# Performance work log

Hardware: AMD Instinct MI355X
Metric: run time of the kernel (lower is better)

## Reference

```python
import jax, jax.numpy as jnp
import numpy as np
from jax import lax

N, C, A, K, D = 2, 256, 3, 20, 256  # batch, channels, anchors, topk person cells, rn_fc_dim
BOX = 4
SIZES = [(80, 128), (40, 64), (20, 32), (10, 16)]
DN = ('NCHW', 'OIHW', 'NCHW')


def _conv(x, w, b):
    return lax.conv_general_dilated(x, w, (1, 1), 'SAME', dimension_numbers=DN) + b[None, :, None, None]


def setup_inputs() -> dict:
    key = jax.random.key(0)
    ks = iter(jax.random.split(key, 40))
    d = {}
    for i, (h, w) in enumerate(SIZES):
        d['feat%d' % i] = jax.random.normal(next(ks), (N, C, h, w), jnp.float32)
    def wfn(shape, s=0.05):
        return jax.random.normal(next(ks), shape, jnp.float32) * s
    d['pc1_w'] = wfn((C, C, 3, 3)); d['pc1_b'] = jnp.zeros((C,), jnp.float32)
    d['pc2_w'] = wfn((C, C, 3, 3)); d['pc2_b'] = jnp.zeros((C,), jnp.float32)
    d['oc1_w'] = wfn((C, C, 3, 3)); d['oc1_b'] = jnp.zeros((C,), jnp.float32)
    d['oc2_w'] = wfn((C, C, 3, 3)); d['oc2_b'] = jnp.zeros((C,), jnp.float32)
    # relation-net FCs: first takes concat(object, person) -> 2C in
    d['rn1_w'] = wfn((D, 2 * C)); d['rn1_b'] = jnp.zeros((D,), jnp.float32)
    d['rn2_w'] = wfn((D, D)); d['rn2_b'] = jnp.zeros((D,), jnp.float32)
    # heads
    d['pl_w'] = wfn((A, C, 1, 1), 0.01); d['pl_b'] = jnp.zeros((A,), jnp.float32)
    d['pd_w'] = wfn((A * BOX, C, 1, 1), 0.01); d['pd_b'] = jnp.zeros((A * BOX,), jnp.float32)
    d['ol_w'] = wfn((A, D), 0.01); d['ol_b'] = jnp.zeros((A,), jnp.float32)
    d['od_w'] = wfn((A * BOX, C, 1, 1), 0.01); d['od_b'] = jnp.zeros((A * BOX,), jnp.float32)
    return d


def _find_top_cells(hidden, logits, topk):
    hid_l, sc_l = [], []
    for h_map, lg in zip(hidden, logits):
        n, c, H, W = h_map.shape
        cell_scores = jnp.max(lg, axis=1).reshape(n, -1)          # (N, HW)
        ts, tc = lax.top_k(cell_scores, topk)                      # (N, K)
        hv = h_map.reshape(n, c, -1)                               # (N, C, HW)
        hid_l.append(jnp.take_along_axis(hv, tc[:, None, :], axis=2))  # (N, C, K)
        sc_l.append(ts)
    scores = jnp.concatenate(sc_l, axis=1)                         # (N, L*K)
    hid = jnp.concatenate(hid_l, axis=2)                           # (N, C, L*K)
    _, keep = lax.top_k(scores, topk)
    return jnp.take_along_axis(hid, keep[:, None, :], axis=2)      # (N, C, K)


def _forward(feats, pc1_w, pc1_b, pc2_w, pc2_b, oc1_w, oc1_b, oc2_w, oc2_b,
             rn1_w, rn1_b, rn2_w, rn2_b, pl_w, pl_b, pd_w, pd_b, ol_w, ol_b, od_w, od_b):
    # person branch
    p_hid, p_log, p_del = [], [], []
    for x in feats:
        x = jax.nn.relu(_conv(x, pc1_w, pc1_b))
        x = jax.nn.relu(_conv(x, pc2_w, pc2_b))
        p_hid.append(x)
        p_log.append(_conv(x, pl_w, pl_b))
        p_del.append(_conv(x, pd_w, pd_b))
    topk_person = _find_top_cells(p_hid, p_log, K)                 # (N, C, K)
    pf = topk_person.transpose(0, 2, 1)                            # (N, K, C)
    # object branch: fc1(concat(o, p)) == o @ Wo.T + p @ Wp.T + b (concat order: object first)
    Wo, Wp = rn1_w[:, :C], rn1_w[:, C:]
    p_proj = jnp.einsum('nkc,dc->nkd', pf, Wp) + rn1_b             # (N, K, D)
    o_log, o_del = [], []
    for x in feats:
        n, _, H, W = x.shape
        y = jax.nn.relu(_conv(x, oc1_w, oc1_b))
        y = jax.nn.relu(_conv(y, oc2_w, oc2_b))
        o_del.append(_conv(y, od_w, od_b))
        yf = y.reshape(n, C, H * W).transpose(0, 2, 1)             # (N, HW, C)
        o_proj = jnp.einsum('nsc,dc->nsd', yf, Wo)                 # (N, HW, D)
        h = jax.nn.relu(o_proj[:, :, None, :] + p_proj[:, None, :, :])  # (N, HW, K, D)
        h = h.sum(axis=2)                                          # (N, HW, D)
        h = jax.nn.relu(jnp.einsum('nsd,ed->nse', h, rn2_w) + rn2_b)
        ol = jnp.einsum('nsd,ad->nsa', h, ol_w) + ol_b             # (N, HW, A)
        o_log.append(ol.transpose(0, 2, 1).reshape(n, A, H, W))
    return tuple(p_log) + tuple(p_del) + tuple(o_log) + tuple(o_del)


def reference(feat0, feat1, feat2, feat3, pc1_w, pc1_b, pc2_w, pc2_b, oc1_w, oc1_b, oc2_w, oc2_b,
              rn1_w, rn1_b, rn2_w, rn2_b, pl_w, pl_b, pd_w, pd_b, ol_w, ol_b, od_w, od_b):
    return _forward([feat0, feat1, feat2, feat3], pc1_w, pc1_b, pc2_w, pc2_b, oc1_w, oc1_b,
                    oc2_w, oc2_b, rn1_w, rn1_b, rn2_w, rn2_b, pl_w, pl_b, pd_w, pd_b,
                    ol_w, ol_b, od_w, od_b)
```

## Files before the change

kernel.cpp:

```cpp
#include <hip/hip_runtime.h>
#include <cstdint>
#include <cstddef>

typedef __bf16 bf16x8 __attribute__((ext_vector_type(8)));
typedef float  f32x16 __attribute__((ext_vector_type(16)));

union U16 { bf16x8 v; uint4 q; };
union U8  { __bf16 h[4]; unsigned long long u; };

typedef __attribute__((address_space(1))) const unsigned char gas_t;
typedef __attribute__((address_space(3))) unsigned char las_t;
__device__ __forceinline__ void async16(const void* g, void* l) {
    __builtin_amdgcn_global_load_lds((gas_t*)g, (las_t*)l, 16, 0, 0);
}

__device__ __forceinline__ int lvl256(int bx) {
    return (bx < 40) ? 0 : (bx < 50) ? 1 : (bx < 53) ? 2 : 3;
}
__device__ __forceinline__ int tbase256(int lv) {
    return (lv == 0) ? 0 : (lv == 1) ? 40 : (lv == 2) ? 50 : 53;
}
__device__ __forceinline__ size_t loffE(int lv) {
    return (lv == 0) ? 0 : (lv == 1) ? 5242880 : (lv == 2) ? 6553600 : 6881280;
}
__device__ __forceinline__ size_t plog_off(int lv) {
    return (lv == 0) ? 0 : (lv == 1) ? 61440 : (lv == 2) ? 76800 : 80640;
}
__device__ __forceinline__ size_t pdel_off(int lv) {
    return (lv == 0) ? 81600 : (lv == 1) ? 327360 : (lv == 2) ? 388800 : 404160;
}
__device__ __forceinline__ size_t olog_off(int lv) {
    return (lv == 0) ? 408000 : (lv == 1) ? 469440 : (lv == 2) ? 484800 : 488640;
}
__device__ __forceinline__ size_t odel_off(int lv) {
    return (lv == 0) ? 489600 : (lv == 1) ? 735360 : (lv == 2) ? 796800 : 812160;
}
__device__ __forceinline__ int soff_l(int lv) {
    return (lv == 0) ? 0 : (lv == 1) ? 20480 : (lv == 2) ? 25600 : 26880;
}

__global__ __launch_bounds__(256) void prep_all_k(
    const float* f0, const float* f1, const float* f2, const float* f3,
    const float* pc1w, const float* pc2w, const float* oc1w, const float* oc2w,
    const float* __restrict__ rn1w, const float* __restrict__ rn2w,
    const float* __restrict__ olw,
    __bf16* __restrict__ wtap, float* __restrict__ WpT,
    __bf16* __restrict__ Wo16, __bf16* __restrict__ rn216,
    __bf16* __restrict__ olw32,
    unsigned* __restrict__ zrow32, __bf16* __restrict__ x16)
{
    __shared__ float f[2304];
    int bid = blockIdx.x, tid = threadIdx.x;
    if (bid < 1024) {
        int which = bid >> 8, co = bid & 255;
        const float* srcw = (which == 0) ? pc1w : (which == 1) ? pc2w
                          : (which == 2) ? oc1w : oc2w;
        const float* src = srcw + (size_t)co * 2304;
        for (int i = tid; i < 2304; i += 256) f[i] = src[i];
        __syncthreads();
        __bf16* dst = wtap + (size_t)which * 589824;
        int cg = co >> 6, co64 = co & 63;
        for (int u = tid; u < 288; u += 256) {
            int t = u >> 5, rest = u & 31, c16 = rest >> 1, hf = rest & 1;
            int ci0 = c16 * 16 + hf * 8;
            U16 v;
#pragma unroll
            for (int j = 0; j < 8; ++j) v.v[j] = (__bf16)f[(ci0 + j) * 9 + t];
            *(uint4*)&dst[(size_t)t * 65536 + c16 * 4096 + cg * 1024 + hf * 512 + co64 * 8] = v.q;
        }
    } else if (bid < 1280) {
        int d = bid - 1024, c = tid;
        WpT[c * 256 + d] = rn1w[(size_t)d * 512 + 256 + c];
        Wo16[((c >> 4) * 256 + d) * 16 + (c & 15)] = (__bf16)rn1w[(size_t)d * 512 + c];
        rn216[((c >> 4) * 256 + d) * 16 + (c & 15)] = (__bf16)rn2w[(size_t)d * 256 + c];
        if (d == 0) zrow32[c] = 0u;
    } else if (bid < 3008) {
        int u = bid - 1280;
        int bx = u >> 5, rr = u & 31, n = rr >> 4, ch = rr & 15;
        int lv = lvl256(bx);
        int HW = 10240 >> (2 * lv);
        int p = (bx - tbase256(lv)) * 256 + tid;
        if (p >= HW) return;
        const float* fp = (lv == 0) ? f0 : (lv == 1) ? f1 : (lv == 2) ? f2 : f3;
        const float* src = fp + (size_t)n * 256 * HW + (size_t)ch * 16 * HW + p;
        U16 a, b;
#pragma unroll
        for (int j = 0; j < 8; ++j) a.v[j] = (__bf16)src[(size_t)j * HW];
#pragma unroll
        for (int j = 0; j < 8; ++j) b.v[j] = (__bf16)src[(size_t)(8 + j) * HW];
        size_t o = loffE(lv) + (size_t)n * HW * 256 + (((size_t)ch * HW + p) << 4);
        *(uint4*)&x16[o] = a.q;
        *(uint4*)&x16[o + 8] = b.q;
    } else {
        int e16 = bid - 3008;
        for (int idx = tid; idx < 512; idx += 256) {
            int co = idx >> 4, j = idx & 15;
            float v = (co < 3) ? olw[co * 256 + e16 * 16 + j] : 0.f;
            olw32[e16 * 512 + co * 16 + j] = (__bf16)v;
        }
    }
}

__global__ __launch_bounds__(256, 3) void conv3x3_v6(
    const __bf16* __restrict__ inA, const __bf16* __restrict__ inB,
    const __bf16* __restrict__ wtA, const __bf16* __restrict__ wtB,
    const float* __restrict__ bA, const float* __restrict__ bB,
    const __bf16* __restrict__ zrow,
    __bf16* __restrict__ outA, __bf16* __restrict__ outB, int mode)
{
    __shared__ __bf16 Asm[2][9216];

    const int id = blockIdx.x;
    const int r8 = id & 7, q = id >> 3;
    int by, br, n, tile;
    if (mode == 0) {
        by = q & 3; br = (q >> 2) & 1;
        int T = ((q >> 3) << 3) + r8; if (T >= 108) return;
        n = T & 1; tile = T >> 1;
    } else if (mode == 1) {
        by = q & 3;
        int T2 = ((q >> 2) << 3) + r8; if (T2 >= 216) return;
        br = T2 & 1; n = (T2 >> 1) & 1; tile = T2 >> 2;
    } else {
        by = q & 3; br = 0;
        int T = ((q >> 2) << 3) + r8; if (T >= 108) return;
        n = T & 1; tile = T >> 1;
    }

    const int tid = threadIdx.x;
    const __bf16* in16 = br ? inB : inA;
    const __bf16* wt = br ? wtB : wtA;
    const float* bias = br ? bB : bA;
    __bf16* outp = br ? outB : outA;

    const int lv = lvl256(tile);
    const int lg2W = 7 - lv;
    const int W = 1 << lg2W, H = 80 >> lv;
    const int HW = 10240 >> (2 * lv);
    const size_t ioff = loffE(lv) + (size_t)n * HW * 256;
    const __bf16* inb = in16 + ioff;

    const int sp0 = (tile - tbase256(lv)) << 8;
    const int npix = min(256, HW - sp0);

    const int w = tid >> 6, l64 = tid & 63;
    const int lane = l64 & 31, half = l64 >> 5;
    const int pix0 = (w << 6) + lane, pix1 = pix0 + 32;
    const int cobase = by << 6;

    int boff0[9], boff1[9];
    {
        const int y0 = sp0 >> lg2W;
        const int py0 = pix0 >> lg2W, px0 = pix0 & (W - 1);
        const int py1 = pix1 >> lg2W, px1 = pix1 & (W - 1);
#pragma unroll
        for (int dy = 0; dy < 3; ++dy)
#pragma unroll
            for (int dx = 0; dx < 3; ++dx) {
                int t = dy * 3 + dx;
                int gy0 = y0 + py0 + dy - 1, gx0 = px0 + dx - 1;
                boff0[t] = ((unsigned)gy0 < (unsigned)H && (unsigned)gx0 < (unsigned)W)
                           ? (((gy0 << lg2W) + gx0) * 32 + half * 16) : -1;
                int gy1 = y0 + py1 + dy - 1, gx1 = px1 + dx - 1;
                boff1[t] = ((unsigned)gy1 < (unsigned)H && (unsigned)gx1 < (unsigned)W)
                           ? (((gy1 << lg2W) + gx1) * 32 + half * 16) : -1;
            }
    }
    const __bf16* zp = zrow + (half << 3);

    const char* wtb = (const char*)wt + (by * 2048);
    auto stage = [&](int c16, int buf) {
        const char* base = wtb + (size_t)c16 * 8192;
        for (int u = w; u < 18; u += 4) {
            int t = u >> 1, hf = u & 1;
            async16(base + (size_t)t * 131072 + hf * 1024 + l64 * 16,
                    &Asm[buf][u * 512]);
        }
    };

    f32x16 acc00 = {}, acc01 = {}, acc10 = {}, acc11 = {};

    stage(0, 0);
    int buf = 0;
    for (int c16 = 0; c16 < 16; ++c16) {
        __syncthreads();
        if (c16 < 15) stage(c16 + 1, buf ^ 1);
        const char* curB = (const char*)inb + (size_t)c16 * HW * 32;
        const __bf16* Ab = &Asm[buf][0];
#pragma unroll
        for (int t = 0; t < 9; ++t) {
            bf16x8 a0 = *(const bf16x8*)&Ab[t * 1024 + half * 512 + lane * 8];
            bf16x8 a1 = *(const bf16x8*)&Ab[t * 1024 + half * 512 + 256 + lane * 8];
            const __bf16* q0 = (boff0[t] >= 0) ? (const __bf16*)(curB + boff0[t]) : zp;
            const __bf16* q1 = (boff1[t] >= 0) ? (const __bf16*)(curB + boff1[t]) : zp;
            bf16x8 b0 = *(const bf16x8*)q0;
            bf16x8 b1 = *(const bf16x8*)q1;
            acc00 = __builtin_amdgcn_mfma_f32_32x32x16_bf16(a0, b0, acc00, 0, 0, 0);
            acc01 = __builtin_amdgcn_mfma_f32_32x32x16_bf16(a0, b1, acc01, 0, 0, 0);
            acc10 = __builtin_amdgcn_mfma_f32_32x32x16_bf16(a1, b0, acc10, 0, 0, 0);
            acc11 = __builtin_amdgcn_mfma_f32_32x32x16_bf16(a1, b1, acc11, 0, 0, 0);
        }
        buf ^= 1;
    }
    const int pixg0 = sp0 + pix0, pixg1 = sp0 + pix1;
    const bool ok0 = (pix0 < npix), ok1 = (pix1 < npix);
#pragma unroll
    for (int b = 0; b < 2; ++b) {
        const f32x16& A0 = b ? acc10 : acc00;
        const f32x16& A1 = b ? acc11 : acc01;
#pragma unroll
        for (int qq = 0; qq < 4; ++qq) {
            int co0 = cobase + b * 32 + qq * 8 + half * 4;
            float4 bq = *(const float4*)&bias[co0];
            U8 v0, v1;
            v0.h[0] = (__bf16)fmaxf(A0[qq * 4 + 0] + bq.x, 0.f);
            v0.h[1] = (__bf16)fmaxf(A0[qq * 4 + 1] + bq.y, 0.f);
            v0.h[2] = (__bf16)fmaxf(A0[qq * 4 + 2] + bq.z, 0.f);
            v0.h[3] = (__bf16)fmaxf(A0[qq * 4 + 3] + bq.w, 0.f);
            v1.h[0] = (__bf16)fmaxf(A1[qq * 4 + 0] + bq.x, 0.f);
            v1.h[1] = (__bf16)fmaxf(A1[qq * 4 + 1] + bq.y, 0.f);
            v1.h[2] = (__bf16)fmaxf(A1[qq * 4 + 2] + bq.z, 0.f);
            v1.h[3] = (__bf16)fmaxf(A1[qq * 4 + 3] + bq.w, 0.f);
            size_t base = ioff + (((size_t)(co0 >> 4) * HW) << 4) + (co0 & 15);
            if (ok0) *(unsigned long long*)&outp[base + ((size_t)pixg0 << 4)] = v0.u;
            if (ok1) *(unsigned long long*)&outp[base + ((size_t)pixg1 << 4)] = v1.u;
        }
    }
}

__global__ __launch_bounds__(256) void heads_k(
    const __bf16* __restrict__ h16p, const __bf16* __restrict__ h16o,
    const float* __restrict__ plw, const float* __restrict__ plb,
    const float* __restrict__ pdw, const float* __restrict__ pdb,
    const float* __restrict__ odw, const float* __restrict__ odb,
    float* __restrict__ out, float* __restrict__ scores)
{
    int bx = blockIdx.x, n = blockIdx.y, br = blockIdx.z;
    int lv = lvl256(bx);
    int HW = 10240 >> (2 * lv);
    int p = (bx - tbase256(lv)) * 256 + threadIdx.x;
    if (p >= HW) return;
    size_t ioff = loffE(lv) + (size_t)n * HW * 256;
    if (br == 0) {
        float acc[15];
#pragma unroll
        for (int a = 0; a < 15; ++a) acc[a] = 0.f;
        for (int ch = 0; ch < 16; ++ch) {
            size_t base = ioff + (((size_t)ch * HW + p) << 4);
            bf16x8 v0 = *(const bf16x8*)&h16p[base];
            bf16x8 v1 = *(const bf16x8*)&h16p[base + 8];
#pragma unroll
            for (int j = 0; j < 16; ++j) {
                float vv = (j < 8) ? (float)v0[j] : (float)v1[j - 8];
                int c = ch * 16 + j;
#pragma unroll
                for (int a = 0; a < 3; ++a)  acc[a]     = fmaf(plw[a * 256 + c], vv, acc[a]);
#pragma unroll
                for (int a = 0; a < 12; ++a) acc[3 + a] = fmaf(pdw[a * 256 + c], vv, acc[3 + a]);
            }
        }
        float sc = -INFINITY;
#pragma unroll
        for (int a = 0; a < 3; ++a) {
            float lg = acc[a] + plb[a];
            out[plog_off(lv) + ((size_t)n * 3 + a) * HW + p] = lg;
            sc = fmaxf(sc, lg);
        }
        scores[soff_l(lv) + (size_t)n * HW + p] = sc;
#pragma unroll
        for (int a = 0; a < 12; ++a)
            out[pdel_off(lv) + ((size_t)n * 12 + a) * HW + p] = acc[3 + a] + pdb[a];
    } else {
        float acc[12];
#pragma unroll
        for (int a = 0; a < 12; ++a) acc[a] = 0.f;
        for (int ch = 0; ch < 16; ++ch) {
            size_t base = ioff + (((size_t)ch * HW + p) << 4);
            bf16x8 v0 = *(const bf16x8*)&h16o[base];
            bf16x8 v1 = *(const bf16x8*)&h16o[base + 8];
#pragma unroll
            for (int j = 0; j < 16; ++j) {
                float vv = (j < 8) ? (float)v0[j] : (float)v1[j - 8];
                int c = ch * 16 + j;
#pragma unroll
                for (int a = 0; a < 12; ++a) acc[a] = fmaf(odw[a * 256 + c], vv, acc[a]);
            }
        }
#pragma unroll
        for (int a = 0; a < 12; ++a)
            out[odel_off(lv) + ((size_t)n * 12 + a) * HW + p] = acc[a] + odb[a];
    }
}

__global__ __launch_bounds__(256) void topk_lvl_k(
    const float* __restrict__ scores, float* __restrict__ lv_sc,
    int* __restrict__ lv_ix)
{
    int l = blockIdx.x, n = blockIdx.y;
    int HW = 10240 >> (2 * l);
    const float* sp = scores + soff_l(l) + (size_t)n * HW;
    int tid = threadIdx.x;
    __shared__ float sc[10240];
    __shared__ float wv4[4];
    __shared__ int wi4[4];
    __shared__ int bcast;
    for (int i = tid; i < HW; i += 256) sc[i] = sp[i];
    __syncthreads();
    float bv = -INFINITY; int bi = 0x7fffffff;
    for (int i = tid; i < HW; i += 256)
        if (sc[i] > bv) { bv = sc[i]; bi = i; }
    const int w = tid >> 6, lane = tid & 63;
    for (int r = 0; r < 20; ++r) {
        float cv = bv; int ci = bi;
#pragma unroll
        for (int off = 32; off > 0; off >>= 1) {
            float ov = __shfl_xor(cv, off);
            int oi = __shfl_xor(ci, off);
            if (ov > cv || (ov == cv && oi < ci)) { cv = ov; ci = oi; }
        }
        if (lane == 0) { wv4[w] = cv; wi4[w] = ci; }
        __syncthreads();
        if (tid == 0) {
            float mv = wv4[0]; int mi = wi4[0];
#pragma unroll
            for (int j = 1; j < 4; ++j)
                if (wv4[j] > mv || (wv4[j] == mv && wi4[j] < mi)) { mv = wv4[j]; mi = wi4[j]; }
            bcast = mi;
            int idx = (n * 4 + l) * 20 + r;
            lv_sc[idx] = mv;
            lv_ix[idx] = mi;
        }
        __syncthreads();
        int mi = bcast;
        if ((mi & 255) == tid) {
            sc[mi] = -INFINITY;
            bv = -INFINITY; bi = 0x7fffffff;
            for (int i = tid; i < HW; i += 256)
                if (sc[i] > bv) { bv = sc[i]; bi = i; }
        }
    }
}

__global__ __launch_bounds__(256) void sel_pproj_k(
    const float* __restrict__ lv_sc, const int* __restrict__ lv_ix,
    const __bf16* __restrict__ h16p, const float* __restrict__ WpT,
    const float* __restrict__ rn1b, float* __restrict__ pp)
{
    int n = blockIdx.x, tid = threadIdx.x;
    __shared__ int selL[20], selC[20];
    __shared__ float pfL[5120];
    __shared__ float wv2[2];
    __shared__ int wi2[2];
    __shared__ int bcast;
    float bv = -INFINITY; int bi = 0x7fffffff;
    if (tid < 80) { bv = lv_sc[n * 80 + tid]; bi = tid; }
    const int w = tid >> 6, lane = tid & 63;
    for (int r = 0; r < 20; ++r) {
        float cv = bv; int ci = bi;
#pragma unroll
        for (int off = 32; off > 0; off >>= 1) {
            float ov = __shfl_xor(cv, off);
            int oi = __shfl_xor(ci, off);
            if (ov > cv || (ov == cv && oi < ci)) { cv = ov; ci = oi; }
        }
        if (lane == 0 && w < 2) { wv2[w] = cv; wi2[w] = ci; }
        __syncthreads();
        if (tid == 0) {
            float mv = wv2[0]; int mi = wi2[0];
            if (wv2[1] > mv || (wv2[1] == mv && wi2[1] < mi)) { mv = wv2[1]; mi = wi2[1]; }
            bcast = mi;
            selL[r] = mi / 20;
            selC[r] = lv_ix[n * 80 + mi];
        }
        __syncthreads();
        if (bcast == bi) bv = -INFINITY;
    }
    for (int t = tid; t < 5120; t += 256) {
        int k = t >> 8, c = t & 255;
        int l = selL[k], cell = selC[k];
        int HW = 10240 >> (2 * l);
        pfL[k * 256 + c] =
            (float)h16p[loffE(l) + (size_t)n * HW * 256 +
                        (((size_t)(c >> 4) * HW + cell) << 4) + (c & 15)];
    }
    __syncthreads();
    float acc[20];
    float bb = rn1b[tid];
#pragma unroll
    for (int k = 0; k < 20; ++k) acc[k] = bb;
    for (int c = 0; c < 256; ++c) {
        float wv = WpT[c * 256 + tid];
#pragma unroll
        for (int k = 0; k < 20; ++k) acc[k] = fmaf(pfL[k * 256 + c], wv, acc[k]);
    }
#pragma unroll
    for (int k = 0; k < 20; ++k)
        pp[(size_t)n * 5120 + k * 256 + tid] = acc[k];
}

__global__ __launch_bounds__(256) void orel_k(
    const __bf16* __restrict__ H16o, const __bf16* __restrict__ Wo16,
    const __bf16* __restrict__ rn216, const __bf16* __restrict__ olw32,
    const float* __restrict__ pp, const float* __restrict__ rn2b,
    const float* __restrict__ olb, float* __restrict__ out)
{
    __shared__ __bf16 hb[16 * 64 * 24];
    __shared__ __bf16 pp16[5120];
    __shared__ float red[768];
    const int tid = threadIdx.x;
    const int n = blockIdx.y;
    int bx = blockIdx.x;
    int lv = (bx < 160) ? 0 : (bx < 200) ? 1 : (bx < 210) ? 2 : 3;
    int tb = (lv == 0) ? 0 : (lv == 1) ? 160 : (lv == 2) ? 200 : 210;
    int HW = 10240 >> (2 * lv);
    size_t yoff = loffE(lv) + (size_t)n * HW * 256;
    int p0 = (bx - tb) << 6;
    int npix = min(64, HW - p0);

    {
        const float* ps = pp + (size_t)n * 5120;
        for (int i = tid; i < 1280; i += 256) {
            float4 f = *(const float4*)&ps[i * 4];
            U8 v;
            v.h[0] = (__bf16)f.x; v.h[1] = (__bf16)f.y;
            v.h[2] = (__bf16)f.z; v.h[3] = (__bf16)f.w;
            *(unsigned long long*)&pp16[i * 4] = v.u;
        }
    }
    __syncthreads();

    const int w = tid >> 6, l64 = tid & 63;
    const int lane = l64 & 31, half = l64 >> 5;
    const int dbase = w << 6;

    f32x16 acc00 = {}, acc01 = {}, acc10 = {}, acc11 = {};
    for (int c16 = 0; c16 < 16; ++c16) {
        bf16x8 a0 = *(const bf16x8*)&Wo16[(((c16 << 8) + dbase + lane) << 4) + (half << 3)];
        bf16x8 a1 = *(const bf16x8*)&Wo16[(((c16 << 8) + dbase + 32 + lane) << 4) + (half << 3)];
        bf16x8 b0 = *(const bf16x8*)&H16o[yoff + (((size_t)c16 * HW + p0 + lane) << 4) + (half << 3)];
        bf16x8 b1 = *(const bf16x8*)&H16o[yoff + (((size_t)c16 * HW + p0 + 32 + lane) << 4) + (half << 3)];
        acc00 = __builtin_amdgcn_mfma_f32_32x32x16_bf16(a0, b0, acc00, 0, 0, 0);
        acc01 = __builtin_amdgcn_mfma_f32_32x32x16_bf16(a0, b1, acc01, 0, 0, 0);
        acc10 = __builtin_amdgcn_mfma_f32_32x32x16_bf16(a1, b0, acc10, 0, 0, 0);
        acc11 = __builtin_amdgcn_mfma_f32_32x32x16_bf16(a1, b1, acc11, 0, 0, 0);
    }
#pragma unroll
    for (int b = 0; b < 2; ++b) {
        const f32x16& A0 = b ? acc10 : acc00;
        const f32x16& A1 = b ? acc11 : acc01;
#pragma unroll
        for (int q = 0; q < 4; ++q) {
            int d0 = dbase + b * 32 + q * 8 + half * 4;
            float h0[4] = {0.f, 0.f, 0.f, 0.f}, h1[4] = {0.f, 0.f, 0.f, 0.f};
            for (int k = 0; k < 20; ++k) {
                U8 pk;
                pk.u = *(const unsigned long long*)&pp16[k * 256 + d0];
#pragma unroll
                for (int j = 0; j < 4; ++j) {
                    float pkv = (float)pk.h[j];
                    h0[j] += fmaxf(A0[q * 4 + j] + pkv, 0.f);
                    h1[j] += fmaxf(A1[q * 4 + j] + pkv, 0.f);
                }
            }
            U8 v0, v1;
#pragma unroll
            for (int j = 0; j < 4; ++j) { v0.h[j] = (__bf16)h0[j]; v1.h[j] = (__bf16)h1[j]; }
            *(unsigned long long*)&hb[((d0 >> 4) * 64 + lane) * 24 + (d0 & 15)] = v0.u;
            *(unsigned long long*)&hb[((d0 >> 4) * 64 + 32 + lane) * 24 + (d0 & 15)] = v1.u;
        }
    }
    __syncthreads();
    f32x16 e00 = {}, e01 = {}, e10 = {}, e11 = {};
    for (int d16 = 0; d16 < 16; ++d16) {
        bf16x8 a0 = *(const bf16x8*)&rn216[(((d16 << 8) + dbase + lane) << 4) + (half << 3)];
        bf16x8 a1 = *(const bf16x8*)&rn216[(((d16 << 8) + dbase + 32 + lane) << 4) + (half << 3)];
        bf16x8 b0 = *(const bf16x8*)&hb[(d16 * 64 + lane) * 24 + (half << 3)];
        bf16x8 b1 = *(const bf16x8*)&hb[(d16 * 64 + 32 + lane) * 24 + (half << 3)];
        e00 = __builtin_amdgcn_mfma_f32_32x32x16_bf16(a0, b0, e00, 0, 0, 0);
        e01 = __builtin_amdgcn_mfma_f32_32x32x16_bf16(a0, b1, e01, 0, 0, 0);
        e10 = __builtin_amdgcn_mfma_f32_32x32x16_bf16(a1, b0, e10, 0, 0, 0);
        e11 = __builtin_amdgcn_mfma_f32_32x32x16_bf16(a1, b1, e11, 0, 0, 0);
    }
    __syncthreads();
#pragma unroll
    for (int b = 0; b < 2; ++b) {
        const f32x16& A0 = b ? e10 : e00;
        const f32x16& A1 = b ? e11 : e01;
#pragma unroll
        for (int q = 0; q < 4; ++q) {
            int e0 = dbase + b * 32 + q * 8 + half * 4;
            float4 bb = *(const float4*)&rn2b[e0];
            U8 v0, v1;
            v0.h[0] = (__bf16)fmaxf(A0[q * 4 + 0] + bb.x, 0.f);
            v0.h[1] = (__bf16)fmaxf(A0[q * 4 + 1] + bb.y, 0.f);
            v0.h[2] = (__bf16)fmaxf(A0[q * 4 + 2] + bb.z, 0.f);
            v0.h[3] = (__bf16)fmaxf(A0[q * 4 + 3] + bb.w, 0.f);
            v1.h[0] = (__bf16)fmaxf(A1[q * 4 + 0] + bb.x, 0.f);
            v1.h[1] = (__bf16)fmaxf(A1[q * 4 + 1] + bb.y, 0.f);
            v1.h[2] = (__bf16)fmaxf(A1[q * 4 + 2] + bb.z, 0.f);
            v1.h[3] = (__bf16)fmaxf(A1[q * 4 + 3] + bb.w, 0.f);
            *(unsigned long long*)&hb[((e0 >> 4) * 64 + lane) * 24 + (e0 & 15)] = v0.u;
            *(unsigned long long*)&hb[((e0 >> 4) * 64 + 32 + lane) * 24 + (e0 & 15)] = v1.u;
        }
    }
    __syncthreads();
    f32x16 ol0 = {}, ol1 = {};
#pragma unroll
    for (int j = 0; j < 4; ++j) {
        int e16 = w * 4 + j;
        bf16x8 a = *(const bf16x8*)&olw32[e16 * 512 + lane * 16 + (half << 3)];
        bf16x8 b0 = *(const bf16x8*)&hb[(e16 * 64 + lane) * 24 + (half << 3)];
        bf16x8 b1 = *(const bf16x8*)&hb[(e16 * 64 + 32 + lane) * 24 + (half << 3)];
        ol0 = __builtin_amdgcn_mfma_f32_32x32x16_bf16(a, b0, ol0, 0, 0, 0);
        ol1 = __builtin_amdgcn_mfma_f32_32x32x16_bf16(a, b1, ol1, 0, 0, 0);
    }
    if (half == 0) {
#pragma unroll
        for (int r = 0; r < 3; ++r) {
            red[(r * 64 + lane) * 4 + w] = ol0[r];
            red[(r * 64 + lane + 32) * 4 + w] = ol1[r];
        }
    }
    __syncthreads();
    if (tid < 192) {
        int a = tid >> 6, px = tid & 63;
        if (px < npix) {
            float4 p4 = *(const float4*)&red[(a * 64 + px) * 4];
            out[olog_off(lv) + ((size_t)n * 3 + a) * HW + p0 + px] =
                olb[a] + p4.x + p4.y + p4.z + p4.w;
        }
    }
}

extern "C" void kernel_launch(void* const* d_in, const int* in_sizes, int n_in,
                              void* d_out, int out_size, void* d_ws, size_t ws_size,
                              hipStream_t stream)
{
    const float* feat[4] = {(const float*)d_in[0], (const float*)d_in[1],
                            (const float*)d_in[2], (const float*)d_in[3]};
    const float* pc1w = (const float*)d_in[4];  const float* pc1b = (const float*)d_in[5];
    const float* pc2w = (const float*)d_in[6];  const float* pc2b = (const float*)d_in[7];
    const float* oc1w = (const float*)d_in[8];  const float* oc1b = (const float*)d_in[9];
    const float* oc2w = (const float*)d_in[10]; const float* oc2b = (const float*)d_in[11];
    const float* rn1w = (const float*)d_in[12]; const float* rn1b = (const float*)d_in[13];
    const float* rn2w = (const float*)d_in[14]; const float* rn2b = (const float*)d_in[15];
    const float* plw  = (const float*)d_in[16]; const float* plb  = (const float*)d_in[17];
    const float* pdw  = (const float*)d_in[18]; const float* pdb  = (const float*)d_in[19];
    const float* olw  = (const float*)d_in[20]; const float* olb  = (const float*)d_in[21];
    const float* odw  = (const float*)d_in[22]; const float* odb  = (const float*)d_in[23];

    float* ws = (float*)d_ws;
    __bf16* bufA = (__bf16*)(ws);
    __bf16* bufB = (__bf16*)(ws + 3481600);
    __bf16* bufC = (__bf16*)(ws + 6963200);
    __bf16* wtap = (__bf16*)(ws + 10444800);
    __bf16* wt_pc1 = wtap;
    __bf16* wt_pc2 = wtap + 589824;
    __bf16* wt_oc1 = wtap + 2 * 589824;
    __bf16* wt_oc2 = wtap + 3 * 589824;
    __bf16* Wo16  = (__bf16*)(ws + 11624448);
    __bf16* rn216 = (__bf16*)(ws + 11657216);
    float* WpT    = ws + 11689984;
    float* scores = ws + 11755520;
    float* lv_sc  = ws + 11783040;
    int*   lv_ix  = (int*)(ws + 11783200);
    __bf16* olw32 = (__bf16*)(ws + 11783360);
    float* pp     = ws + 11793280;
    __bf16* zrow  = (__bf16*)(ws + 11803520);
    __bf16* bufD  = (__bf16*)(ws + 11803904);
    float* out    = (float*)d_out;

    const bool merged = ws_size >= (size_t)(11803904 + 3481600) * 4;

    hipLaunchKernelGGL(prep_all_k, dim3(3024), dim3(256), 0, stream,
                       feat[0], feat[1], feat[2], feat[3],
                       pc1w, pc2w, oc1w, oc2w, rn1w, rn2w, olw,
                       wtap, WpT, Wo16, rn216, olw32, (unsigned*)zrow, bufA);

    hipLaunchKernelGGL(conv3x3_v6, dim3(896), dim3(256), 0, stream,
                       bufA, bufA, wt_pc1, wt_oc1, pc1b, oc1b, zrow,
                       bufB, bufC, 0);

    __bf16* h16o;
    if (merged) {
        hipLaunchKernelGGL(conv3x3_v6, dim3(864), dim3(256), 0, stream,
                           bufB, bufC, wt_pc2, wt_oc2, pc2b, oc2b, zrow,
                           bufA, bufD, 1);
        h16o = bufD;
    } else {
        hipLaunchKernelGGL(conv3x3_v6, dim3(448), dim3(256), 0, stream,
                           bufB, bufB, wt_pc2, wt_pc2, pc2b, pc2b, zrow,
                           bufA, bufA, 2);
        hipLaunchKernelGGL(conv3x3_v6, dim3(448), dim3(256), 0, stream,
                           bufC, bufC, wt_oc2, wt_oc2, oc2b, oc2b, zrow,
                           bufB, bufB, 2);
        h16o = bufB;
    }

    hipLaunchKernelGGL(heads_k, dim3(54, 2, 2), dim3(256), 0, stream,
                       bufA, h16o, plw, plb, pdw, pdb, odw, odb, out, scores);

    hipLaunchKernelGGL(topk_lvl_k, dim3(4, 2), dim3(256), 0, stream,
                       scores, lv_sc, lv_ix);
    hipLaunchKernelGGL(sel_pproj_k, dim3(2), dim3(256), 0, stream,
                       lv_sc, lv_ix, bufA, WpT, rn1b, pp);

    hipLaunchKernelGGL(orel_k, dim3(213, 2), dim3(256), 0, stream,
                       h16o, Wo16, rn216, olw32, pp, rn2b, olb, out);
}
```

Before: 497.2 us.

## Fuse object delta head into orel kernel via MFMA and raise conv occupancy hint

The object-branch 1x1 delta head moves out of the scalar-FMA heads kernel and into orel_k. There it runs as extra MFMA ops on the same activation fragments already loaded for the Wo projection, using a new bf16 padded weight buffer built in prep. This removes a second full read of the object hidden map and halves the heads grid. Separately, the conv launch bound goes from 3 to 4 waves, which may force register spills. The delta head now runs in bf16 inside a single warp, so that warp does more work than the others.

```diff
diff --git a/kernel.cpp b/kernel.cpp
--- a/kernel.cpp
+++ b/kernel.cpp
@@ -43,10 +43,10 @@
     const float* f0, const float* f1, const float* f2, const float* f3,
     const float* pc1w, const float* pc2w, const float* oc1w, const float* oc2w,
     const float* __restrict__ rn1w, const float* __restrict__ rn2w,
-    const float* __restrict__ olw,
+    const float* __restrict__ olw, const float* __restrict__ odw,
     __bf16* __restrict__ wtap, float* __restrict__ WpT,
     __bf16* __restrict__ Wo16, __bf16* __restrict__ rn216,
-    __bf16* __restrict__ olw32,
+    __bf16* __restrict__ olw32, __bf16* __restrict__ odw32,
     unsigned* __restrict__ zrow32, __bf16* __restrict__ x16)
 {
     __shared__ float f[2304];
@@ -91,17 +91,24 @@
         size_t o = loffE(lv) + (size_t)n * HW * 256 + (((size_t)ch * HW + p) << 4);
         *(uint4*)&x16[o] = a.q;
         *(uint4*)&x16[o + 8] = b.q;
-    } else {
+    } else if (bid < 3024) {
         int e16 = bid - 3008;
         for (int idx = tid; idx < 512; idx += 256) {
             int co = idx >> 4, j = idx & 15;
             float v = (co < 3) ? olw[co * 256 + e16 * 16 + j] : 0.f;
             olw32[e16 * 512 + co * 16 + j] = (__bf16)v;
         }
-    }
-}
-
-__global__ __launch_bounds__(256, 3) void conv3x3_v6(
+    } else {
+        int c16 = bid - 3024;
+        for (int idx = tid; idx < 512; idx += 256) {
+            int co = idx >> 4, j = idx & 15;
+            float v = (co < 12) ? odw[co * 256 + c16 * 16 + j] : 0.f;
+            odw32[c16 * 512 + co * 16 + j] = (__bf16)v;
+        }
+    }
+}
+
+__global__ __launch_bounds__(256, 4) void conv3x3_v6(
     const __bf16* __restrict__ inA, const __bf16* __restrict__ inB,
     const __bf16* __restrict__ wtA, const __bf16* __restrict__ wtB,
     const float* __restrict__ bA, const float* __restrict__ bB,
@@ -229,67 +236,45 @@
 }
 
 __global__ __launch_bounds__(256) void heads_k(
-    const __bf16* __restrict__ h16p, const __bf16* __restrict__ h16o,
+    const __bf16* __restrict__ h16p,
     const float* __restrict__ plw, const float* __restrict__ plb,
     const float* __restrict__ pdw, const float* __restrict__ pdb,
-    const float* __restrict__ odw, const float* __restrict__ odb,
     float* __restrict__ out, float* __restrict__ scores)
 {
-    int bx = blockIdx.x, n = blockIdx.y, br = blockIdx.z;
+    int bx = blockIdx.x, n = blockIdx.y;
     int lv = lvl256(bx);
     int HW = 10240 >> (2 * lv);
     int p = (bx - tbase256(lv)) * 256 + threadIdx.x;
     if (p >= HW) return;
     size_t ioff = loffE(lv) + (size_t)n * HW * 256;
-    if (br == 0) {
-        float acc[15];
-#pragma unroll
-        for (int a = 0; a < 15; ++a) acc[a] = 0.f;
-        for (int ch = 0; ch < 16; ++ch) {
-            size_t base = ioff + (((size_t)ch * HW + p) << 4);
-            bf16x8 v0 = *(const bf16x8*)&h16p[base];
-            bf16x8 v1 = *(const bf16x8*)&h16p[base + 8];
-#pragma unroll
-            for (int j = 0; j < 16; ++j) {
-                float vv = (j < 8) ? (float)v0[j] : (float)v1[j - 8];
-                int c = ch * 16 + j;
-#pragma unroll
-                for (int a = 0; a < 3; ++a)  acc[a]     = fmaf(plw[a * 256 + c], vv, acc[a]);
-#pragma unroll
-                for (int a = 0; a < 12; ++a) acc[3 + a] = fmaf(pdw[a * 256 + c], vv, acc[3 + a]);
-            }
-        }
-        float sc = -INFINITY;
-#pragma unroll
-        for (int a = 0; a < 3; ++a) {
-            float lg = acc[a] + plb[a];
-            out[plog_off(lv) + ((size_t)n * 3 + a) * HW + p] = lg;
-            sc = fmaxf(sc, lg);
-        }
-        scores[soff_l(lv) + (size_t)n * HW + p] = sc;
-#pragma unroll
-        for (int a = 0; a < 12; ++a)
-            out[pdel_off(lv) + ((size_t)n * 12 + a) * HW + p] = acc[3 + a] + pdb[a];
-    } else {
-        float acc[12];
-#pragma unroll
-        for (int a = 0; a < 12; ++a) acc[a] = 0.f;
-        for (int ch = 0; ch < 16; ++ch) {
-            size_t base = ioff + (((size_t)ch * HW + p) << 4);
-            bf16x8 v0 = *(const bf16x8*)&h16o[base];
-            bf16x8 v1 = *(const bf16x8*)&h16o[base + 8];
-#pragma unroll
-            for (int j = 0; j < 16; ++j) {
-                float vv = (j < 8) ? (float)v0[j] : (float)v1[j - 8];
-                int c = ch * 16 + j;
-#pragma unroll
-                for (int a = 0; a < 12; ++a) acc[a] = fmaf(odw[a * 256 + c], vv, acc[a]);
-            }
-        }
-#pragma unroll
-        for (int a = 0; a < 12; ++a)
-            out[odel_off(lv) + ((size_t)n * 12 + a) * HW + p] = acc[a] + odb[a];
-    }
+    float acc[15];
+#pragma unroll
+    for (int a = 0; a < 15; ++a) acc[a] = 0.f;
+    for (int ch = 0; ch < 16; ++ch) {
+        size_t base = ioff + (((size_t)ch * HW + p) << 4);
+        bf16x8 v0 = *(const bf16x8*)&h16p[base];
+        bf16x8 v1 = *(const bf16x8*)&h16p[base + 8];
+#pragma unroll
+        for (int j = 0; j < 16; ++j) {
+            float vv = (j < 8) ? (float)v0[j] : (float)v1[j - 8];
+            int c = ch * 16 + j;
+#pragma unroll
+            for (int a = 0; a < 3; ++a)  acc[a]     = fmaf(plw[a * 256 + c], vv, acc[a]);
+#pragma unroll
+            for (int a = 0; a < 12; ++a) acc[3 + a] = fmaf(pdw[a * 256 + c], vv, acc[3 + a]);
+        }
+    }
+    float sc = -INFINITY;
+#pragma unroll
+    for (int a = 0; a < 3; ++a) {
+        float lg = acc[a] + plb[a];
+        out[plog_off(lv) + ((size_t)n * 3 + a) * HW + p] = lg;
+        sc = fmaxf(sc, lg);
+    }
+    scores[soff_l(lv) + (size_t)n * HW + p] = sc;
+#pragma unroll
+    for (int a = 0; a < 12; ++a)
+        out[pdel_off(lv) + ((size_t)n * 12 + a) * HW + p] = acc[3 + a] + pdb[a];
 }
 
 __global__ __launch_bounds__(256) void topk_lvl_k(
@@ -401,8 +386,9 @@
 __global__ __launch_bounds__(256) void orel_k(
     const __bf16* __restrict__ H16o, const __bf16* __restrict__ Wo16,
     const __bf16* __restrict__ rn216, const __bf16* __restrict__ olw32,
-    const float* __restrict__ pp, const float* __restrict__ rn2b,
-    const float* __restrict__ olb, float* __restrict__ out)
+    const __bf16* __restrict__ odw32, const float* __restrict__ pp,
+    const float* __restrict__ rn2b, const float* __restrict__ olb,
+    const float* __restrict__ odb, float* __restrict__ out)
 {
     __shared__ __bf16 hb[16 * 64 * 24];
     __shared__ __bf16 pp16[5120];
@@ -434,6 +420,7 @@
     const int dbase = w << 6;
 
     f32x16 acc00 = {}, acc01 = {}, acc10 = {}, acc11 = {};
+    f32x16 od0 = {}, od1 = {};
     for (int c16 = 0; c16 < 16; ++c16) {
         bf16x8 a0 = *(const bf16x8*)&Wo16[(((c16 << 8) + dbase + lane) << 4) + (half << 3)];
         bf16x8 a1 = *(const bf16x8*)&Wo16[(((c16 << 8) + dbase + 32 + lane) << 4) + (half << 3)];
@@ -443,6 +430,23 @@
         acc01 = __builtin_amdgcn_mfma_f32_32x32x16_bf16(a0, b1, acc01, 0, 0, 0);
         acc10 = __builtin_amdgcn_mfma_f32_32x32x16_bf16(a1, b0, acc10, 0, 0, 0);
         acc11 = __builtin_amdgcn_mfma_f32_32x32x16_bf16(a1, b1, acc11, 0, 0, 0);
+        if (w == 0) {
+            bf16x8 ao = *(const bf16x8*)&odw32[(c16 << 9) + lane * 16 + (half << 3)];
+            od0 = __builtin_amdgcn_mfma_f32_32x32x16_bf16(ao, b0, od0, 0, 0, 0);
+            od1 = __builtin_amdgcn_mfma_f32_32x32x16_bf16(ao, b1, od1, 0, 0, 0);
+        }
+    }
+    if (w == 0) {
+        size_t ob = odel_off(lv) + (size_t)n * 12 * HW + p0;
+#pragma unroll
+        for (int reg = 0; reg < 16; ++reg) {
+            int row = (reg & 3) + ((reg >> 2) << 3) + (half << 2);
+            if (row < 12) {
+                float bv = odb[row];
+                if (lane < npix)      out[ob + (size_t)row * HW + lane] = od0[reg] + bv;
+                if (32 + lane < npix) out[ob + (size_t)row * HW + 32 + lane] = od1[reg] + bv;
+            }
+        }
     }
 #pragma unroll
     for (int b = 0; b < 2; ++b) {
@@ -565,6 +569,7 @@
     float* lv_sc  = ws + 11783040;
     int*   lv_ix  = (int*)(ws + 11783200);
     __bf16* olw32 = (__bf16*)(ws + 11783360);
+    __bf16* odw32 = (__bf16*)(ws + 11787456);
     float* pp     = ws + 11793280;
     __bf16* zrow  = (__bf16*)(ws + 11803520);
     __bf16* bufD  = (__bf16*)(ws + 11803904);
@@ -572,10 +577,10 @@
 
     const bool merged = ws_size >= (size_t)(11803904 + 3481600) * 4;
 
-    hipLaunchKernelGGL(prep_all_k, dim3(3024), dim3(256), 0, stream,
+    hipLaunchKernelGGL(prep_all_k, dim3(3040), dim3(256), 0, stream,
                        feat[0], feat[1], feat[2], feat[3],
-                       pc1w, pc2w, oc1w, oc2w, rn1w, rn2w, olw,
-                       wtap, WpT, Wo16, rn216, olw32, (unsigned*)zrow, bufA);
+                       pc1w, pc2w, oc1w, oc2w, rn1w, rn2w, olw, odw,
+                       wtap, WpT, Wo16, rn216, olw32, odw32, (unsigned*)zrow, bufA);
 
     hipLaunchKernelGGL(conv3x3_v6, dim3(896), dim3(256), 0, stream,
                        bufA, bufA, wt_pc1, wt_oc1, pc1b, oc1b, zrow,
@@ -597,8 +602,8 @@
         h16o = bufB;
     }
 
-    hipLaunchKernelGGL(heads_k, dim3(54, 2, 2), dim3(256), 0, stream,
-                       bufA, h16o, plw, plb, pdw, pdb, odw, odb, out, scores);
+    hipLaunchKernelGGL(heads_k, dim3(54, 2), dim3(256), 0, stream,
+                       bufA, plw, plb, pdw, pdb, out, scores);
 
     hipLaunchKernelGGL(topk_lvl_k, dim3(4, 2), dim3(256), 0, stream,
                        scores, lv_sc, lv_ix);
@@ -606,5 +611,5 @@
                        lv_sc, lv_ix, bufA, WpT, rn1b, pp);
 
     hipLaunchKernelGGL(orel_k, dim3(213, 2), dim3(256), 0, stream,
-                       h16o, Wo16, rn216, olw32, pp, rn2b, olb, out);
-}
+                       h16o, Wo16, rn216, olw32, odw32, pp, rn2b, olb, odb, out);
+}
```

After: 528.2 us. 6.2% more time.
